# Kernel optimization log

Measured on AMD Instinct MI355X. Metric: run time of the kernel, lower is better.

Reference implementation:

```python
import jax, jax.numpy as jnp
import numpy as np

B, L = 2, 2048
D_MODEL, D_INNER, D_STATE, DT_RANK = 512, 1024, 16, 32
N_LAYERS, BLOCK, N_HEADS, CONV_K = 15, 64, 4, 4
VOCAB, D_OUT = 32000, 512


def setup_inputs() -> dict:
    key = jax.random.key(0)
    ks = iter(jax.random.split(key, 40))
    def nrm(shape, s=0.02):
        return jax.random.normal(next(ks), shape, dtype=jnp.float32) * s
    return {
        "tokens": jax.random.randint(next(ks), (B, L), 0, VOCAB, dtype=jnp.int32),
        "embed": nrm((VOCAB, D_MODEL)),
        "rms_w": jnp.ones((N_LAYERS, D_MODEL), jnp.float32),
        "W_in": nrm((N_LAYERS, D_MODEL, 2 * D_INNER)),
        "conv_w": nrm((N_LAYERS, D_INNER, CONV_K), 0.1),
        "conv_b": jnp.zeros((N_LAYERS, D_INNER), jnp.float32),
        "x_proj": nrm((N_LAYERS, D_INNER, DT_RANK + 2 * D_STATE)),
        "dt_w": nrm((N_LAYERS, DT_RANK, D_INNER), 0.1),
        "dt_b": jnp.full((N_LAYERS, D_INNER), -2.0, jnp.float32),
        "A_log": jnp.log(jnp.broadcast_to(jnp.arange(1, D_STATE + 1, dtype=jnp.float32), (N_LAYERS, D_INNER, D_STATE)) + 0.0),
        "D_skip": jnp.ones((N_LAYERS, D_INNER), jnp.float32),
        "W_out": nrm((N_LAYERS, D_INNER, D_MODEL)),
        "init_state": jnp.zeros((N_LAYERS, 1, 1, D_MODEL), jnp.float32),
        "Wq": nrm((D_MODEL, D_MODEL)), "Wk": nrm((D_MODEL, D_MODEL)), "Wv": nrm((D_MODEL, D_MODEL)),
        "bq": jnp.zeros((D_MODEL,), jnp.float32), "bk": jnp.zeros((D_MODEL,), jnp.float32), "bv": jnp.zeros((D_MODEL,), jnp.float32),
        "Wo_attn": nrm((D_MODEL, D_MODEL)), "bo": jnp.zeros((D_MODEL,), jnp.float32),
        "ln_w": jnp.ones((D_MODEL,), jnp.float32), "ln_b": jnp.zeros((D_MODEL,), jnp.float32),
        "head_w": nrm((D_MODEL, D_OUT)),
    }


def _silu(x):
    return x * jax.nn.sigmoid(x)


def _rmsnorm(x, w, eps=1e-6):
    return x * jax.lax.rsqrt(jnp.mean(x * x, axis=-1, keepdims=True) + eps) * w


def _mamba_block(h, Wi, cw, cb, xpw, dtw, dtb, Alog, Dsk, Wo):
    # h: (B, T, D) with T = BLOCK + 1 (state token prepended)
    Bb, T, _ = h.shape
    x, z = jnp.split(h @ Wi, 2, axis=-1)                      # (B,T,di) each
    xpad = jnp.pad(x, ((0, 0), (CONV_K - 1, 0), (0, 0)))      # causal depthwise conv
    x = sum(xpad[:, k:k + T, :] * cw[:, k] for k in range(CONV_K)) + cb
    x = _silu(x)
    xdbl = x @ xpw                                            # (B,T,dt_rank+2*ds)
    dt = jax.nn.softplus(xdbl[..., :DT_RANK] @ dtw + dtb)     # (B,T,di)
    Bt = xdbl[..., DT_RANK:DT_RANK + D_STATE]                 # (B,T,ds)
    Ct = xdbl[..., DT_RANK + D_STATE:]                        # (B,T,ds)
    A = -jnp.exp(Alog)                                        # (di,ds)

    def step(s, inp):
        dt_t, B_t, C_t, x_t = inp                             # (B,di),(B,ds),(B,ds),(B,di)
        s = s * jnp.exp(dt_t[..., None] * A) + (dt_t * x_t)[..., None] * B_t[:, None, :]
        return s, jnp.einsum('bds,bs->bd', s, C_t)

    s0 = jnp.zeros((Bb, D_INNER, D_STATE), x.dtype)
    xs = tuple(a.transpose(1, 0, 2) for a in (dt, Bt, Ct, x))  # time-major
    _, ys = jax.lax.scan(step, s0, xs)
    y = ys.transpose(1, 0, 2) + Dsk * x
    return (y * _silu(z)) @ Wo


def reference(tokens, embed, rms_w, W_in, conv_w, conv_b, x_proj, dt_w, dt_b,
              A_log, D_skip, W_out, init_state, Wq, Wk, Wv, bq, bk, bv,
              Wo_attn, bo, ln_w, ln_b, head_w):
    h = embed[tokens]                                          # (B,L,D)
    nB = L // BLOCK
    chunks = h.reshape(B, nB, BLOCK, D_MODEL).transpose(1, 0, 2, 3)  # (nB,B,bs,D)
    states0 = jnp.broadcast_to(init_state, (N_LAYERS, B, 1, D_MODEL)) + 0.0

    def block_step(states, chunk):
        co = chunk
        new_states = []
        for j in range(N_LAYERS):
            cwc = jnp.concatenate([states[j], _rmsnorm(co, rms_w[j])], axis=1)
            lo = _mamba_block(cwc, W_in[j], conv_w[j], conv_b[j], x_proj[j],
                              dt_w[j], dt_b[j], A_log[j], D_skip[j], W_out[j])
            new_states.append(jax.lax.stop_gradient(lo[:, -1:, :]))
            co = co + lo[:, 1:, :]
        ns = jnp.stack(new_states)
        return ns, (co, ns[-1][:, 0, :])

    _, (out_chunks, mem) = jax.lax.scan(block_step, states0, chunks)
    mamba_out = out_chunks.transpose(1, 0, 2, 3).reshape(B, L, D_MODEL)
    memory_bank = mem.transpose(1, 0, 2)                       # (B,nB,D)

    dh = D_MODEL // N_HEADS
    q = (mamba_out @ Wq.T + bq).reshape(B, L, N_HEADS, dh)
    k = (memory_bank @ Wk.T + bk).reshape(B, nB, N_HEADS, dh)
    v = (memory_bank @ Wv.T + bv).reshape(B, nB, N_HEADS, dh)
    tb = jnp.arange(L) // BLOCK
    allowed = jnp.arange(nB)[None, :] < tb[:, None]            # (L,nB) strictly-past blocks
    has_past = tb > 0
    mask = jnp.where(allowed | ~has_past[:, None], 0.0, -1e9)
    scores = jnp.einsum('blhd,bmhd->bhlm', q, k) / float(np.sqrt(dh)) + mask
    attn = jax.nn.softmax(scores, axis=-1)
    ao = jnp.einsum('bhlm,bmhd->blhd', attn, v).reshape(B, L, D_MODEL)
    ao = (ao @ Wo_attn.T + bo) * has_past.astype(mamba_out.dtype)[None, :, None]

    hres = mamba_out + ao
    mu = jnp.mean(hres, axis=-1, keepdims=True)
    var = jnp.var(hres, axis=-1, keepdims=True)
    hf = (hres - mu) * jax.lax.rsqrt(var + 1e-5) * ln_w + ln_b
    return hf @ head_w
```

## Files before the change

kernel.cpp:

```cpp
#include <hip/hip_runtime.h>
#include <hip/hip_cooperative_groups.h>

namespace cg = cooperative_groups;

typedef unsigned short u16;
typedef unsigned int u32;
typedef __attribute__((ext_vector_type(8))) short bf16x8;
typedef __attribute__((ext_vector_type(4))) float f32x4;

constexpr int BATCH = 2, SEQL = 2048, DMODEL = 512, DINNER = 1024;
constexpr int NLAYER = 15, BLKSZ = 64, NCHUNK = 32, TT = 65;

constexpr size_t OFF_H   = 0;
constexpr size_t OFF_ST  = 2097152;
constexpr size_t OFF_MEM = 2112512;
constexpr size_t OFF_XZ  = 2145280;
constexpr size_t OFF_XC  = 6138880;
constexpr size_t OFF_ANB = 8135680;
constexpr size_t OFF_XCB = 8688640;
constexpr size_t OFF_YMB = 9917440;
constexpr size_t OFF_WIT = 10900480;
constexpr size_t OFF_WOT = 18764800;
constexpr size_t OFF_XPT = 22696960;
constexpr size_t OFF_Q   = 2145280;
constexpr size_t OFF_K   = 4242432;
constexpr size_t OFF_V   = 4275200;
constexpr size_t OFF_AO  = 4307968;
constexpr size_t OFF_WTA = 6405120;

__device__ __forceinline__ u16 f2b(float f) {
  u32 u = __builtin_bit_cast(u32, f);
  u = (u + 0x7fffu + ((u >> 16) & 1u)) >> 16;
  return (u16)u;
}
__device__ __forceinline__ u32 pk2(float a, float b) {
  return (u32)f2b(a) | ((u32)f2b(b) << 16);
}

__global__ void __launch_bounds__(256,2)
wtrans_k(const float* __restrict__ src, u16* __restrict__ dst,
         int R, int C, int tiles_rc, int tc)
{
  __shared__ float tile[64*65];
  const int mat = blockIdx.x / tiles_rc;
  const int rem = blockIdx.x % tiles_rc;
  const int r0 = (rem / tc) * 64, c0 = (rem % tc) * 64;
  const float* s = src + (size_t)mat * R * C;
  u16* d = dst + (size_t)mat * C * R;
  for (int i = threadIdx.x; i < 4096; i += 256) {
    const int r = i >> 6, cc = i & 63;
    tile[r*65 + cc] = s[(size_t)(r0 + r)*C + c0 + cc];
  }
  __syncthreads();
  for (int i = threadIdx.x; i < 4096; i += 256) {
    const int ci = i >> 6, rr = i & 63;
    d[(size_t)(c0 + ci)*R + r0 + rr] = f2b(tile[rr*65 + ci]);
  }
}

__global__ void __launch_bounds__(256, 2)
mamba_coop(const int* __restrict__ tokens, const float* __restrict__ embed,
           const float* __restrict__ rms_w, const float* __restrict__ conv_w,
           const float* __restrict__ conv_b, const float* __restrict__ dt_w,
           const float* __restrict__ dt_b, const float* __restrict__ A_log,
           const float* __restrict__ D_skip, const float* __restrict__ init_state,
           float* __restrict__ ws)
{
  cg::grid_group grid = cg::this_grid();
  __shared__ __align__(16) float xd_lds[80*64];
  float* h_  = ws + OFF_H;
  float* st_ = ws + OFF_ST;
  float* memb = ws + OFF_MEM;
  const int NWG = gridDim.x;
  const int wg = blockIdx.x, tid = threadIdx.x;
  const int wv = tid >> 6, ln = tid & 63;
  const int lr = ln & 15, lq = ln >> 4;

  {
    const int gtid = wg*256 + tid;
    const int gstr = NWG*256;
    for (int g = gtid; g < BATCH*SEQL*(DMODEL/8); g += gstr) {
      const int bl = g >> 6;
      const int m0 = (g & 63) << 3;
      const int tok = tokens[bl];
      const float* ep = embed + (size_t)tok*DMODEL + m0;
      float* hp = h_ + (size_t)bl*DMODEL + m0;
      *(float4*)hp     = *(const float4*)ep;
      *(float4*)(hp+4) = *(const float4*)(ep+4);
    }
    for (int i = gtid; i < NLAYER*BATCH*DMODEL; i += gstr) {
      const int m = i & (DMODEL-1);
      const int j = i / (BATCH*DMODEL);
      st_[i] = init_state[j*DMODEL + m];
    }
  }
  grid.sync();

  for (int diag = 0; diag < NCHUNK + NLAYER - 1; ++diag) {
    const int c_lo = (diag - (NLAYER-1)) > 0 ? (diag - (NLAYER-1)) : 0;
    const int c_hi = diag < (NCHUNK-1) ? diag : (NCHUNK-1);
    const int nst = c_hi - c_lo + 1;
    const int sidx = wg % nst;
    const int swg  = wg / nst;
    const int nwg  = (NWG - 1 - sidx)/nst + 1;
    const int c = c_lo + sidx;
    const int j = diag - c;
    float* xz  = ws + OFF_XZ + (size_t)j*266240;
    float* xcf = ws + OFF_XC + (size_t)j*133120;
    u16* anb = (u16*)(ws + OFF_ANB) + (size_t)j*73728;
    u16* xcb = (u16*)(ws + OFF_XCB) + (size_t)j*163840;
    u16* ymb = (u16*)(ws + OFF_YMB) + (size_t)j*131072;
    const u16* WiT = (const u16*)(ws + OFF_WIT) + (size_t)j*1048576;
    const u16* WoT = (const u16*)(ws + OFF_WOT) + (size_t)j*524288;
    const u16* XpT = (const u16*)(ws + OFF_XPT) + (size_t)j*65536;
    const float* rw = rms_w + (size_t)j*DMODEL;

    {
      const int nwaves = nwg*4;
      for (int m = swg*4 + wv; m < 144; m += nwaves) {
        const int k0 = ln*8;
        uint4 pk;
        if (m < 130) {
          const int b = m/TT, t = m - b*TT;
          float v[8];
          if (t == 0) {
            const float* sp = st_ + ((size_t)j*BATCH + b)*DMODEL + k0;
            #pragma unroll
            for (int x = 0; x < 8; ++x) v[x] = sp[x];
          } else {
            const float* hp = h_ + (size_t)(b*SEQL + c*BLKSZ + t-1)*DMODEL + k0;
            const float4 v0 = *(const float4*)hp;
            const float4 v1 = *(const float4*)(hp+4);
            float ss = v0.x*v0.x + v0.y*v0.y + v0.z*v0.z + v0.w*v0.w
                     + v1.x*v1.x + v1.y*v1.y + v1.z*v1.z + v1.w*v1.w;
            #pragma unroll
            for (int off = 32; off > 0; off >>= 1) ss += __shfl_xor(ss, off);
            const float rs = rsqrtf(ss * (1.f/512.f) + 1e-6f);
            const float o[8] = {v0.x,v0.y,v0.z,v0.w,v1.x,v1.y,v1.z,v1.w};
            #pragma unroll
            for (int x = 0; x < 8; ++x) v[x] = o[x] * rs * rw[k0 + x];
          }
          pk = make_uint4(pk2(v[0],v[1]), pk2(v[2],v[3]), pk2(v[4],v[5]), pk2(v[6],v[7]));
        } else {
          pk = make_uint4(0,0,0,0);
        }
        *(uint4*)(anb + (size_t)m*512 + k0) = pk;
      }
    }
    grid.sync();

    {
      const float* cvb = conv_b + (size_t)j*DINNER;
      const float* cww = conv_w + (size_t)j*DINNER*4;
      for (int nb = swg; nb < 32; nb += nwg) {
        const int n_base = nb*64;
        f32x4 acc[3][4] = {};
        for (int kk = 0; kk < 16; ++kk) {
          const int k0 = kk*32 + lq*8;
          bf16x8 bf[4];
          #pragma unroll
          for (int nt = 0; nt < 4; ++nt)
            bf[nt] = *(const bf16x8*)(WiT + (size_t)(n_base + nt*16 + lr)*512 + k0);
          #pragma unroll
          for (int i = 0; i < 3; ++i) {
            if (i == 2 && wv != 0) continue;
            const int mt = wv + 4*i;
            const bf16x8 af = *(const bf16x8*)(anb + (size_t)(mt*16 + lr)*512 + k0);
            #pragma unroll
            for (int nt = 0; nt < 4; ++nt)
              acc[i][nt] = __builtin_amdgcn_mfma_f32_16x16x32_bf16(af, bf[nt], acc[i][nt], 0, 0, 0);
          }
        }
        #pragma unroll
        for (int i = 0; i < 3; ++i) {
          if (i == 2 && wv != 0) continue;
          const int mt = wv + 4*i;
          #pragma unroll
          for (int nt = 0; nt < 4; ++nt)
            #pragma unroll
            for (int r = 0; r < 4; ++r) {
              const int m = mt*16 + lq*4 + r;
              if (m < 130)
                xz[(size_t)m*2048 + n_base + nt*16 + lr] = acc[i][nt][r];
            }
        }
        if (nb < 16) {
          __syncthreads();
          for (int e = tid; e < 64*160; e += 256) {
            const int d = n_base + (e & 63);
            const int row2 = e >> 6;
            const int b = row2 / 80, t = row2 - b*80;
            if (t < TT) {
              const int m = b*TT + t;
              float a = cvb[d];
              #pragma unroll
              for (int q = 0; q < 4; ++q) {
                const int tt = t - 3 + q;
                if (tt >= 0) a = fmaf(xz[(size_t)(b*TT+tt)*2048 + d], cww[d*4+q], a);
              }
              const float sv = a / (1.f + __expf(-a));
              xcf[(size_t)m*1024 + d] = sv;
              xcb[(size_t)row2*1024 + d] = f2b(sv);
            } else {
              xcb[(size_t)row2*1024 + d] = 0;
            }
          }
        }
      }
    }
    grid.sync();

    if (swg < 8) {
      const int p = swg, b = p >> 2;
      const u16* xa = xcb + (size_t)b*80*1024;
      for (int mt = 0; mt < 5; ++mt) {
        f32x4 acc = {};
        for (int kk = 0; kk < 32; ++kk) {
          const int k0 = kk*32 + lq*8;
          const bf16x8 af = *(const bf16x8*)(xa + (size_t)(mt*16 + lr)*1024 + k0);
          const bf16x8 bf = *(const bf16x8*)(XpT + (size_t)(wv*16 + lr)*1024 + k0);
          acc = __builtin_amdgcn_mfma_f32_16x16x32_bf16(af, bf, acc, 0, 0, 0);
        }
        #pragma unroll
        for (int r = 0; r < 4; ++r)
          xd_lds[(mt*16 + lq*4 + r)*64 + wv*16 + lr] = acc[r];
      }
      __syncthreads();
      const int d = (p & 3)*256 + tid;
      float dtwr[32];
      const float* dwp = dt_w + (size_t)j*32*DINNER + d;
      #pragma unroll
      for (int r = 0; r < 32; ++r) dtwr[r] = dwp[(size_t)r*DINNER];
      float Ai[16], s[16];
      const float* alp = A_log + (size_t)j*DINNER*16 + (size_t)d*16;
      #pragma unroll
      for (int i = 0; i < 16; ++i) { Ai[i] = -__expf(alp[i]); s[i] = 0.f; }
      const float dtbv = dt_b[(size_t)j*DINNER + d];
      const float Dv   = D_skip[(size_t)j*DINNER + d];
      for (int t = 0; t < TT; ++t) {
        const float4* row = (const float4*)(xd_lds + t*64);
        float dl = dtbv;
        #pragma unroll
        for (int r = 0; r < 8; ++r) {
          const float4 x = row[r];
          dl = fmaf(x.x, dtwr[4*r+0], dl);
          dl = fmaf(x.y, dtwr[4*r+1], dl);
          dl = fmaf(x.z, dtwr[4*r+2], dl);
          dl = fmaf(x.w, dtwr[4*r+3], dl);
        }
        const float e = __expf(dl);
        const float dtv = (dl > 15.f) ? dl : log1pf(e);
        const float xcv = xcf[(size_t)(b*TT+t)*1024 + d];
        const float u = dtv * xcv;
        float yv = 0.f;
        #pragma unroll
        for (int i = 0; i < 4; ++i) {
          const float4 Bv = row[8+i];
          const float4 Cv = row[12+i];
          float P;
          P = __expf(dtv*Ai[4*i+0]); s[4*i+0] = fmaf(s[4*i+0], P, u*Bv.x); yv = fmaf(s[4*i+0], Cv.x, yv);
          P = __expf(dtv*Ai[4*i+1]); s[4*i+1] = fmaf(s[4*i+1], P, u*Bv.y); yv = fmaf(s[4*i+1], Cv.y, yv);
          P = __expf(dtv*Ai[4*i+2]); s[4*i+2] = fmaf(s[4*i+2], P, u*Bv.z); yv = fmaf(s[4*i+2], Cv.z, yv);
          P = __expf(dtv*Ai[4*i+3]); s[4*i+3] = fmaf(s[4*i+3], P, u*Bv.w); yv = fmaf(s[4*i+3], Cv.w, yv);
        }
        const float zv = xz[(size_t)(b*TT+t)*2048 + 1024 + d];
        const float sz = zv / (1.f + __expf(-zv));
        if (t >= 1)
          ymb[(size_t)(b*64 + t-1)*1024 + d] = f2b((yv + Dv*xcv) * sz);
      }
    }
    grid.sync();

    {
      for (int nt0 = swg; nt0 < 32; nt0 += nwg) {
        f32x4 acc[2] = {};
        for (int kk = 0; kk < 32; ++kk) {
          const int k0 = kk*32 + lq*8;
          const bf16x8 bf = *(const bf16x8*)(WoT + (size_t)(nt0*16 + lr)*1024 + k0);
          #pragma unroll
          for (int i = 0; i < 2; ++i) {
            const int mt = wv*2 + i;
            const bf16x8 af = *(const bf16x8*)(ymb + (size_t)(mt*16 + lr)*1024 + k0);
            acc[i] = __builtin_amdgcn_mfma_f32_16x16x32_bf16(af, bf, acc[i], 0, 0, 0);
          }
        }
        const int col = nt0*16 + lr;
        #pragma unroll
        for (int i = 0; i < 2; ++i) {
          const int mt = wv*2 + i;
          #pragma unroll
          for (int r = 0; r < 4; ++r) {
            const int m = mt*16 + lq*4 + r;
            const int b = m >> 6, tm = m & 63;
            const float v = acc[i][r];
            float* hp = h_ + (size_t)(b*SEQL + c*BLKSZ + tm)*DMODEL + col;
            *hp += v;
            if (tm == 63) {
              st_[((size_t)j*BATCH + b)*DMODEL + col] = v;
              if (j == NLAYER-1)
                memb[((size_t)b*NCHUNK + c)*DMODEL + col] = v;
            }
          }
        }
      }
    }
    grid.sync();
  }
}

__global__ void __launch_bounds__(256,1)
transpose_k(const float* __restrict__ wq, const float* __restrict__ wk,
            const float* __restrict__ wvm, const float* __restrict__ wo,
            float* __restrict__ ws)
{
  float* wt = ws + OFF_WTA;
  const float* srcs[4] = { wq, wk, wvm, wo };
  const int which = blockIdx.x >> 10;
  const int idx = ((blockIdx.x & 1023) << 8) + threadIdx.x;
  const int o = idx >> 9, m = idx & 511;
  wt[(size_t)which*262144 + (size_t)m*512 + o] = srcs[which][(size_t)o*512 + m];
}

__global__ void __launch_bounds__(256,1)
qkv_k(const float* __restrict__ bq, const float* __restrict__ bk, const float* __restrict__ bv,
      float* __restrict__ ws)
{
  __shared__ __align__(16) float lds[8192];
  const float* wt = ws + OFF_WTA;
  const int wg = blockIdx.x, tid = threadIdx.x;
  const int rtg = wg >> 2, ct = wg & 3;
  const float* A; const float* Bm; const float* bias; float* out; int m0;
  if (rtg < 256)      { A = ws+OFF_H;   Bm = wt;          bias = bq; out = ws+OFF_Q; m0 = rtg*16; }
  else if (rtg < 260) { A = ws+OFF_MEM; Bm = wt + 262144; bias = bk; out = ws+OFF_K; m0 = (rtg-256)*16; }
  else                { A = ws+OFF_MEM; Bm = wt + 524288; bias = bv; out = ws+OFF_V; m0 = (rtg-260)*16; }
  for (int i = tid; i < 2048; i += 256) {
    const int f = i*4;
    *(float4*)(lds+f) = *(const float4*)(A + (size_t)(m0 + (f>>9))*512 + (f & 511));
  }
  __syncthreads();
  const int col0 = ct*128 + (tid & 63)*2;
  const int rq = tid >> 6;
  const float2* wp2 = (const float2*)(Bm + col0);
  const float* ap = lds + rq*2048;
  float acc0[4] = {0,0,0,0}, acc1[4] = {0,0,0,0};
  for (int k = 0; k < 512; k += 4) {
    const float2 w0 = wp2[(size_t)(k+0)*256];
    const float2 w1 = wp2[(size_t)(k+1)*256];
    const float2 w2 = wp2[(size_t)(k+2)*256];
    const float2 w3 = wp2[(size_t)(k+3)*256];
    #pragma unroll
    for (int r4 = 0; r4 < 4; ++r4) {
      const float4 a = *(const float4*)(ap + r4*512 + k);
      acc0[r4] = fmaf(a.x, w0.x, acc0[r4]); acc1[r4] = fmaf(a.x, w0.y, acc1[r4]);
      acc0[r4] = fmaf(a.y, w1.x, acc0[r4]); acc1[r4] = fmaf(a.y, w1.y, acc1[r4]);
      acc0[r4] = fmaf(a.z, w2.x, acc0[r4]); acc1[r4] = fmaf(a.z, w2.y, acc1[r4]);
      acc0[r4] = fmaf(a.w, w3.x, acc0[r4]); acc1[r4] = fmaf(a.w, w3.y, acc1[r4]);
    }
  }
  const float bb0 = bias[col0], bb1 = bias[col0+1];
  #pragma unroll
  for (int r4 = 0; r4 < 4; ++r4)
    *(float2*)(out + (size_t)(m0 + rq*4 + r4)*512 + col0) = make_float2(acc0[r4]+bb0, acc1[r4]+bb1);
}

__global__ void __launch_bounds__(256,1)
attn_k(float* __restrict__ ws)
{
  const float* q  = ws + OFF_Q;
  const float* kk = ws + OFF_K;
  const float* vvv = ws + OFF_V;
  float* ao = ws + OFF_AO;
  const int gw = (blockIdx.x*256 + threadIdx.x) >> 6;
  const int ln = threadIdx.x & 63;
  const int l = gw & (SEQL-1);
  const int bh = gw >> 11;
  const int b = bh >> 2, hh = bh & 3;
  const int tb = l >> 6;
  float* aop = ao + (size_t)(b*SEQL + l)*512 + hh*128;
  if (tb == 0) { *(float2*)(aop + ln*2) = make_float2(0.f, 0.f); return; }
  float sc = -1e30f;
  if (ln < tb) {
    const float* qp = q + (size_t)(b*SEQL+l)*512 + hh*128;
    const float* kp = kk + (size_t)(b*NCHUNK+ln)*512 + hh*128;
    float s = 0.f;
    for (int dd = 0; dd < 128; dd += 4) {
      const float4 qq = *(const float4*)(qp+dd);
      const float4 kv = *(const float4*)(kp+dd);
      s += qq.x*kv.x + qq.y*kv.y + qq.z*kv.z + qq.w*kv.w;
    }
    sc = s * 0.08838834764831845f;
  }
  float mx = sc;
  #pragma unroll
  for (int off = 32; off > 0; off >>= 1) mx = fmaxf(mx, __shfl_xor(mx, off));
  const float w = (ln < tb) ? __expf(sc - mx) : 0.f;
  float sm = w;
  #pragma unroll
  for (int off = 32; off > 0; off >>= 1) sm += __shfl_xor(sm, off);
  const float inv = 1.f / sm;
  float a0 = 0.f, a1 = 0.f;
  const int d0 = ln*2;
  for (int mm = 0; mm < tb; ++mm) {
    const float am = __shfl(w, mm) * inv;
    const float2 vp = *(const float2*)(vvv + (size_t)(b*NCHUNK+mm)*512 + hh*128 + d0);
    a0 = fmaf(am, vp.x, a0);
    a1 = fmaf(am, vp.y, a1);
  }
  *(float2*)(aop + d0) = make_float2(a0, a1);
}

__global__ void __launch_bounds__(256,1)
outproj_k(const float* __restrict__ bo, float* __restrict__ ws)
{
  __shared__ __align__(16) float lds[8192];
  float* ao  = ws + OFF_AO;
  const float* woT = ws + OFF_WTA + 786432;
  const float* h_ = ws + OFF_H;
  const int wg = blockIdx.x, tid = threadIdx.x;
  const int rtg = wg >> 2, ct = wg & 3;
  const int m0 = rtg*16;
  for (int i = tid; i < 2048; i += 256) {
    const int f = i*4;
    *(float4*)(lds+f) = *(const float4*)(ao + (size_t)(m0 + (f>>9))*512 + (f & 511));
  }
  __syncthreads();
  const int col0 = ct*128 + (tid & 63)*2;
  const int rq = tid >> 6;
  const float2* wp2 = (const float2*)(woT + col0);
  const float* ap = lds + rq*2048;
  float acc0[4] = {0,0,0,0}, acc1[4] = {0,0,0,0};
  for (int k = 0; k < 512; k += 4) {
    const float2 w0 = wp2[(size_t)(k+0)*256];
    const float2 w1 = wp2[(size_t)(k+1)*256];
    const float2 w2 = wp2[(size_t)(k+2)*256];
    const float2 w3 = wp2[(size_t)(k+3)*256];
    #pragma unroll
    for (int r4 = 0; r4 < 4; ++r4) {
      const float4 a = *(const float4*)(ap + r4*512 + k);
      acc0[r4] = fmaf(a.x, w0.x, acc0[r4]); acc1[r4] = fmaf(a.x, w0.y, acc1[r4]);
      acc0[r4] = fmaf(a.y, w1.x, acc0[r4]); acc1[r4] = fmaf(a.y, w1.y, acc1[r4]);
      acc0[r4] = fmaf(a.z, w2.x, acc0[r4]); acc1[r4] = fmaf(a.z, w2.y, acc1[r4]);
      acc0[r4] = fmaf(a.w, w3.x, acc0[r4]); acc1[r4] = fmaf(a.w, w3.y, acc1[r4]);
    }
  }
  const float bb0 = bo[col0], bb1 = bo[col0+1];
  #pragma unroll
  for (int r4 = 0; r4 < 4; ++r4) {
    const int m = m0 + rq*4 + r4;
    const float hp = ((m & (SEQL-1)) >= BLKSZ) ? 1.f : 0.f;
    const float2 hv = *(const float2*)(h_ + (size_t)m*512 + col0);
    *(float2*)(ao + (size_t)m*512 + col0) =
        make_float2(hv.x + (acc0[r4]+bb0)*hp, hv.y + (acc1[r4]+bb1)*hp);
  }
}

__global__ void __launch_bounds__(256,1)
lnhead_k(const float* __restrict__ lnw, const float* __restrict__ lnb,
         const float* __restrict__ head_w, float* __restrict__ ws, float* __restrict__ out)
{
  __shared__ __align__(16) float lds[8192];
  const float* hres = ws + OFF_AO;
  const int wg = blockIdx.x, tid = threadIdx.x;
  const int wv = tid >> 6, ln = tid & 63;
  const int rtg = wg >> 2, ct = wg & 3;
  const int m0 = rtg*16;
  for (int r = wv; r < 16; r += 4) {
    const float* src = hres + (size_t)(m0+r)*512 + ln*8;
    const float4 v0 = *(const float4*)src;
    const float4 v1 = *(const float4*)(src+4);
    float s1 = v0.x+v0.y+v0.z+v0.w + v1.x+v1.y+v1.z+v1.w;
    float s2 = v0.x*v0.x+v0.y*v0.y+v0.z*v0.z+v0.w*v0.w
             + v1.x*v1.x+v1.y*v1.y+v1.z*v1.z+v1.w*v1.w;
    #pragma unroll
    for (int off = 32; off > 0; off >>= 1) { s1 += __shfl_xor(s1, off); s2 += __shfl_xor(s2, off); }
    const float mu = s1 * (1.f/512.f);
    const float var = fmaxf(s2 * (1.f/512.f) - mu*mu, 0.f);
    const float nf = rsqrtf(var + 1e-5f);
    const float o[8] = {v0.x,v0.y,v0.z,v0.w,v1.x,v1.y,v1.z,v1.w};
    #pragma unroll
    for (int x = 0; x < 8; ++x)
      lds[r*512 + ln*8 + x] = (o[x]-mu)*nf*lnw[ln*8+x] + lnb[ln*8+x];
  }
  __syncthreads();
  const int col0 = ct*128 + (tid & 63)*2;
  const int rq = tid >> 6;
  const float2* wp2 = (const float2*)(head_w + col0);
  const float* ap = lds + rq*2048;
  float acc0[4] = {0,0,0,0}, acc1[4] = {0,0,0,0};
  for (int k = 0; k < 512; k += 4) {
    const float2 w0 = wp2[(size_t)(k+0)*256];
    const float2 w1 = wp2[(size_t)(k+1)*256];
    const float2 w2 = wp2[(size_t)(k+2)*256];
    const float2 w3 = wp2[(size_t)(k+3)*256];
    #pragma unroll
    for (int r4 = 0; r4 < 4; ++r4) {
      const float4 a = *(const float4*)(ap + r4*512 + k);
      acc0[r4] = fmaf(a.x, w0.x, acc0[r4]); acc1[r4] = fmaf(a.x, w0.y, acc1[r4]);
      acc0[r4] = fmaf(a.y, w1.x, acc0[r4]); acc1[r4] = fmaf(a.y, w1.y, acc1[r4]);
      acc0[r4] = fmaf(a.z, w2.x, acc0[r4]); acc1[r4] = fmaf(a.z, w2.y, acc1[r4]);
      acc0[r4] = fmaf(a.w, w3.x, acc0[r4]); acc1[r4] = fmaf(a.w, w3.y, acc1[r4]);
    }
  }
  #pragma unroll
  for (int r4 = 0; r4 < 4; ++r4) {
    const size_t oi = (size_t)(m0 + rq*4 + r4)*512 + col0;
    *(float2*)(out + oi) = make_float2(acc0[r4], acc1[r4]);
  }
}

extern "C" void kernel_launch(void* const* d_in, const int* in_sizes, int n_in,
                              void* d_out, int out_size, void* d_ws, size_t ws_size,
                              hipStream_t stream)
{
  const int*   tokens     = (const int*)d_in[0];
  const float* embed      = (const float*)d_in[1];
  const float* rms_w      = (const float*)d_in[2];
  const float* W_in       = (const float*)d_in[3];
  const float* conv_w     = (const float*)d_in[4];
  const float* conv_b     = (const float*)d_in[5];
  const float* x_proj     = (const float*)d_in[6];
  const float* dt_w       = (const float*)d_in[7];
  const float* dt_b       = (const float*)d_in[8];
  const float* A_log      = (const float*)d_in[9];
  const float* D_skip     = (const float*)d_in[10];
  const float* W_out      = (const float*)d_in[11];
  const float* init_state = (const float*)d_in[12];
  const float* Wq         = (const float*)d_in[13];
  const float* Wk         = (const float*)d_in[14];
  const float* Wv         = (const float*)d_in[15];
  const float* bq         = (const float*)d_in[16];
  const float* bk         = (const float*)d_in[17];
  const float* bv         = (const float*)d_in[18];
  const float* Wo_attn    = (const float*)d_in[19];
  const float* bo         = (const float*)d_in[20];
  const float* ln_w       = (const float*)d_in[21];
  const float* ln_b       = (const float*)d_in[22];
  const float* head_w     = (const float*)d_in[23];
  float* ws = (float*)d_ws;
  float* out = (float*)d_out;

  hipLaunchKernelGGL(wtrans_k, dim3(15*8*32), dim3(256), 0, stream,
                     W_in, (u16*)(ws + OFF_WIT), 512, 2048, 8*32, 32);
  hipLaunchKernelGGL(wtrans_k, dim3(15*16*8), dim3(256), 0, stream,
                     W_out, (u16*)(ws + OFF_WOT), 1024, 512, 16*8, 8);
  hipLaunchKernelGGL(wtrans_k, dim3(15*16*1), dim3(256), 0, stream,
                     x_proj, (u16*)(ws + OFF_XPT), 1024, 64, 16*1, 1);

  int occ = 1;
  (void)hipOccupancyMaxActiveBlocksPerMultiprocessor(&occ, mamba_coop, 256, 0);
  if (occ < 1) occ = 1;
  if (occ > 2) occ = 2;
  const int grid = 256 * occ;

  void* args[] = { (void*)&tokens, (void*)&embed, (void*)&rms_w,
                   (void*)&conv_w, (void*)&conv_b, (void*)&dt_w,
                   (void*)&dt_b, (void*)&A_log, (void*)&D_skip,
                   (void*)&init_state, (void*)&ws };
  hipLaunchCooperativeKernel(reinterpret_cast<const void*>(&mamba_coop),
                             dim3(grid), dim3(256), args, 0, stream);

  hipLaunchKernelGGL(transpose_k, dim3(4096), dim3(256), 0, stream, Wq, Wk, Wv, Wo_attn, ws);
  hipLaunchKernelGGL(qkv_k, dim3(1056), dim3(256), 0, stream, bq, bk, bv, ws);
  hipLaunchKernelGGL(attn_k, dim3(4096), dim3(256), 0, stream, ws);
  hipLaunchKernelGGL(outproj_k, dim3(1024), dim3(256), 0, stream, bo, ws);
  hipLaunchKernelGGL(lnhead_k, dim3(1024), dim3(256), 0, stream, ln_w, ln_b, head_w, ws, out);
}
```

Before: 15.94 ms.

## Replace grid-wide syncs with per-layer workgroup groups and flag-based dataflow

```diff
diff --git a/kernel.cpp b/kernel.cpp
--- a/kernel.cpp
+++ b/kernel.cpp
@@ -1,7 +1,4 @@
 #include <hip/hip_runtime.h>
-#include <hip/hip_cooperative_groups.h>
-
-namespace cg = cooperative_groups;
 
 typedef unsigned short u16;
 typedef unsigned int u32;
@@ -10,18 +7,20 @@
 
 constexpr int BATCH = 2, SEQL = 2048, DMODEL = 512, DINNER = 1024;
 constexpr int NLAYER = 15, BLKSZ = 64, NCHUNK = 32, TT = 65;
+constexpr int NWG = 480;
 
 constexpr size_t OFF_H   = 0;
 constexpr size_t OFF_ST  = 2097152;
 constexpr size_t OFF_MEM = 2112512;
 constexpr size_t OFF_XZ  = 2145280;
-constexpr size_t OFF_XC  = 6138880;
-constexpr size_t OFF_ANB = 8135680;
-constexpr size_t OFF_XCB = 8688640;
-constexpr size_t OFF_YMB = 9917440;
-constexpr size_t OFF_WIT = 10900480;
-constexpr size_t OFF_WOT = 18764800;
-constexpr size_t OFF_XPT = 22696960;
+constexpr size_t OFF_ANB = 6138880;
+constexpr size_t OFF_XCB = 6691840;
+constexpr size_t OFF_YMB = 7920640;
+constexpr size_t OFF_WIT = 8903680;
+constexpr size_t OFF_WOT = 16768000;
+constexpr size_t OFF_XPT = 20700160;
+constexpr size_t OFF_DTW = 21191680;
+constexpr size_t OFF_FLG = 21437440;
 constexpr size_t OFF_Q   = 2145280;
 constexpr size_t OFF_K   = 4242432;
 constexpr size_t OFF_V   = 4275200;
@@ -33,8 +32,34 @@
   u = (u + 0x7fffu + ((u >> 16) & 1u)) >> 16;
   return (u16)u;
 }
+__device__ __forceinline__ float b2f(u16 u) {
+  u32 v = ((u32)u) << 16;
+  return __builtin_bit_cast(float, v);
+}
 __device__ __forceinline__ u32 pk2(float a, float b) {
   return (u32)f2b(a) | ((u32)f2b(b) << 16);
+}
+
+__device__ __forceinline__ void spin_until(int* f, int target) {
+  int k = 0;
+  while (__hip_atomic_load(f, __ATOMIC_RELAXED, __HIP_MEMORY_SCOPE_AGENT) < target) {
+    __builtin_amdgcn_s_sleep(8);
+    if (((++k) & 255) == 0)
+      (void)__hip_atomic_load(f, __ATOMIC_ACQUIRE, __HIP_MEMORY_SCOPE_AGENT);
+  }
+  (void)__hip_atomic_load(f, __ATOMIC_ACQUIRE, __HIP_MEMORY_SCOPE_AGENT);
+}
+__device__ __forceinline__ void wait_flag(int* f, int target) {
+  if (threadIdx.x == 0) spin_until(f, target);
+  __syncthreads();
+}
+__device__ __forceinline__ void stage_bar(int* f, int target, bool arrive) {
+  __syncthreads();
+  if (threadIdx.x == 0) {
+    if (arrive) __hip_atomic_fetch_add(f, 1, __ATOMIC_RELEASE, __HIP_MEMORY_SCOPE_AGENT);
+    spin_until(f, target);
+  }
+  __syncthreads();
 }
 
 __global__ void __launch_bounds__(256,2)
@@ -58,23 +83,32 @@
   }
 }
 
+__global__ void __launch_bounds__(256,2)
+dtwtrans_k(const float* __restrict__ src, u16* __restrict__ dst)
+{
+  const int i = blockIdx.x*256 + threadIdx.x;
+  const int jj = i >> 15, rem = i & 32767;
+  const int d = rem >> 5, r = rem & 31;
+  dst[i] = f2b(src[(size_t)jj*32768 + (size_t)r*1024 + d]);
+}
+
 __global__ void __launch_bounds__(256, 2)
 mamba_coop(const int* __restrict__ tokens, const float* __restrict__ embed,
            const float* __restrict__ rms_w, const float* __restrict__ conv_w,
-           const float* __restrict__ conv_b, const float* __restrict__ dt_w,
-           const float* __restrict__ dt_b, const float* __restrict__ A_log,
-           const float* __restrict__ D_skip, const float* __restrict__ init_state,
-           float* __restrict__ ws)
-{
-  cg::grid_group grid = cg::this_grid();
+           const float* __restrict__ conv_b, const float* __restrict__ dt_b,
+           const float* __restrict__ A_log, const float* __restrict__ D_skip,
+           const float* __restrict__ init_state, float* __restrict__ ws)
+{
   __shared__ __align__(16) float xd_lds[80*64];
   float* h_  = ws + OFF_H;
   float* st_ = ws + OFF_ST;
   float* memb = ws + OFF_MEM;
-  const int NWG = gridDim.x;
+  int* FLG = (int*)(ws + OFF_FLG);
   const int wg = blockIdx.x, tid = threadIdx.x;
   const int wv = tid >> 6, ln = tid & 63;
   const int lr = ln & 15, lq = ln >> 4;
+  const int j = wg >> 5;
+  const int swg = wg & 31;
 
   {
     const int gtid = wg*256 + tid;
@@ -90,128 +124,117 @@
     }
     for (int i = gtid; i < NLAYER*BATCH*DMODEL; i += gstr) {
       const int m = i & (DMODEL-1);
-      const int j = i / (BATCH*DMODEL);
-      st_[i] = init_state[j*DMODEL + m];
-    }
-  }
-  grid.sync();
-
-  for (int diag = 0; diag < NCHUNK + NLAYER - 1; ++diag) {
-    const int c_lo = (diag - (NLAYER-1)) > 0 ? (diag - (NLAYER-1)) : 0;
-    const int c_hi = diag < (NCHUNK-1) ? diag : (NCHUNK-1);
-    const int nst = c_hi - c_lo + 1;
-    const int sidx = wg % nst;
-    const int swg  = wg / nst;
-    const int nwg  = (NWG - 1 - sidx)/nst + 1;
-    const int c = c_lo + sidx;
-    const int j = diag - c;
-    float* xz  = ws + OFF_XZ + (size_t)j*266240;
-    float* xcf = ws + OFF_XC + (size_t)j*133120;
-    u16* anb = (u16*)(ws + OFF_ANB) + (size_t)j*73728;
-    u16* xcb = (u16*)(ws + OFF_XCB) + (size_t)j*163840;
-    u16* ymb = (u16*)(ws + OFF_YMB) + (size_t)j*131072;
-    const u16* WiT = (const u16*)(ws + OFF_WIT) + (size_t)j*1048576;
-    const u16* WoT = (const u16*)(ws + OFF_WOT) + (size_t)j*524288;
-    const u16* XpT = (const u16*)(ws + OFF_XPT) + (size_t)j*65536;
-    const float* rw = rms_w + (size_t)j*DMODEL;
+      const int jj = i / (BATCH*DMODEL);
+      st_[i] = init_state[jj*DMODEL + m];
+    }
+  }
+  stage_bar(FLG + 30720, NWG, true);
+
+  float* xz  = ws + OFF_XZ + (size_t)j*266240;
+  u16* anb = (u16*)(ws + OFF_ANB) + (size_t)j*73728;
+  u16* xcb = (u16*)(ws + OFF_XCB) + (size_t)j*163840;
+  u16* ymb = (u16*)(ws + OFF_YMB) + (size_t)j*131072;
+  const u16* WiT = (const u16*)(ws + OFF_WIT) + (size_t)j*1048576;
+  const u16* WoT = (const u16*)(ws + OFF_WOT) + (size_t)j*524288;
+  const u16* XpT = (const u16*)(ws + OFF_XPT) + (size_t)j*65536;
+  const u16* DwT = (const u16*)(ws + OFF_DTW) + (size_t)j*32768;
+  const float* rw = rms_w + (size_t)j*DMODEL;
+  const float* cvb = conv_b + (size_t)j*DINNER;
+  const float* cww = conv_w + (size_t)j*DINNER*4;
+
+  for (int c = 0; c < NCHUNK; ++c) {
+    int* fs = FLG + ((c*15 + j)*4)*16;
+    if (j > 0) wait_flag(FLG + ((c*15 + j-1)*4 + 3)*16, 32);
+
+    for (int m = swg*4 + wv; m < 144; m += 128) {
+      const int k0 = ln*8;
+      uint4 pk;
+      if (m < 130) {
+        const int b = m/TT, t = m - b*TT;
+        float v[8];
+        if (t == 0) {
+          const float* sp = st_ + ((size_t)j*BATCH + b)*DMODEL + k0;
+          #pragma unroll
+          for (int x = 0; x < 8; ++x) v[x] = sp[x];
+        } else {
+          const float* hp = h_ + (size_t)(b*SEQL + c*BLKSZ + t-1)*DMODEL + k0;
+          const float4 v0 = *(const float4*)hp;
+          const float4 v1 = *(const float4*)(hp+4);
+          float ss = v0.x*v0.x + v0.y*v0.y + v0.z*v0.z + v0.w*v0.w
+                   + v1.x*v1.x + v1.y*v1.y + v1.z*v1.z + v1.w*v1.w;
+          #pragma unroll
+          for (int off = 32; off > 0; off >>= 1) ss += __shfl_xor(ss, off);
+          const float rs = rsqrtf(ss * (1.f/512.f) + 1e-6f);
+          const float o[8] = {v0.x,v0.y,v0.z,v0.w,v1.x,v1.y,v1.z,v1.w};
+          #pragma unroll
+          for (int x = 0; x < 8; ++x) v[x] = o[x] * rs * rw[k0 + x];
+        }
+        pk = make_uint4(pk2(v[0],v[1]), pk2(v[2],v[3]), pk2(v[4],v[5]), pk2(v[6],v[7]));
+      } else {
+        pk = make_uint4(0,0,0,0);
+      }
+      *(uint4*)(anb + (size_t)m*512 + k0) = pk;
+    }
+    stage_bar(fs + 0*16, 32, true);
 
     {
-      const int nwaves = nwg*4;
-      for (int m = swg*4 + wv; m < 144; m += nwaves) {
-        const int k0 = ln*8;
-        uint4 pk;
-        if (m < 130) {
-          const int b = m/TT, t = m - b*TT;
-          float v[8];
-          if (t == 0) {
-            const float* sp = st_ + ((size_t)j*BATCH + b)*DMODEL + k0;
-            #pragma unroll
-            for (int x = 0; x < 8; ++x) v[x] = sp[x];
-          } else {
-            const float* hp = h_ + (size_t)(b*SEQL + c*BLKSZ + t-1)*DMODEL + k0;
-            const float4 v0 = *(const float4*)hp;
-            const float4 v1 = *(const float4*)(hp+4);
-            float ss = v0.x*v0.x + v0.y*v0.y + v0.z*v0.z + v0.w*v0.w
-                     + v1.x*v1.x + v1.y*v1.y + v1.z*v1.z + v1.w*v1.w;
-            #pragma unroll
-            for (int off = 32; off > 0; off >>= 1) ss += __shfl_xor(ss, off);
-            const float rs = rsqrtf(ss * (1.f/512.f) + 1e-6f);
-            const float o[8] = {v0.x,v0.y,v0.z,v0.w,v1.x,v1.y,v1.z,v1.w};
-            #pragma unroll
-            for (int x = 0; x < 8; ++x) v[x] = o[x] * rs * rw[k0 + x];
-          }
-          pk = make_uint4(pk2(v[0],v[1]), pk2(v[2],v[3]), pk2(v[4],v[5]), pk2(v[6],v[7]));
-        } else {
-          pk = make_uint4(0,0,0,0);
-        }
-        *(uint4*)(anb + (size_t)m*512 + k0) = pk;
-      }
-    }
-    grid.sync();
-
-    {
-      const float* cvb = conv_b + (size_t)j*DINNER;
-      const float* cww = conv_w + (size_t)j*DINNER*4;
-      for (int nb = swg; nb < 32; nb += nwg) {
-        const int n_base = nb*64;
-        f32x4 acc[3][4] = {};
-        for (int kk = 0; kk < 16; ++kk) {
-          const int k0 = kk*32 + lq*8;
-          bf16x8 bf[4];
-          #pragma unroll
-          for (int nt = 0; nt < 4; ++nt)
-            bf[nt] = *(const bf16x8*)(WiT + (size_t)(n_base + nt*16 + lr)*512 + k0);
-          #pragma unroll
-          for (int i = 0; i < 3; ++i) {
-            if (i == 2 && wv != 0) continue;
-            const int mt = wv + 4*i;
-            const bf16x8 af = *(const bf16x8*)(anb + (size_t)(mt*16 + lr)*512 + k0);
-            #pragma unroll
-            for (int nt = 0; nt < 4; ++nt)
-              acc[i][nt] = __builtin_amdgcn_mfma_f32_16x16x32_bf16(af, bf[nt], acc[i][nt], 0, 0, 0);
-          }
-        }
+      const int nb = swg;
+      const int n_base = nb*64;
+      f32x4 acc[3][4] = {};
+      for (int kk = 0; kk < 16; ++kk) {
+        const int k0 = kk*32 + lq*8;
+        bf16x8 bf[4];
+        #pragma unroll
+        for (int nt = 0; nt < 4; ++nt)
+          bf[nt] = *(const bf16x8*)(WiT + (size_t)(n_base + nt*16 + lr)*512 + k0);
         #pragma unroll
         for (int i = 0; i < 3; ++i) {
           if (i == 2 && wv != 0) continue;
           const int mt = wv + 4*i;
+          const bf16x8 af = *(const bf16x8*)(anb + (size_t)(mt*16 + lr)*512 + k0);
           #pragma unroll
           for (int nt = 0; nt < 4; ++nt)
+            acc[i][nt] = __builtin_amdgcn_mfma_f32_16x16x32_bf16(af, bf[nt], acc[i][nt], 0, 0, 0);
+        }
+      }
+      #pragma unroll
+      for (int i = 0; i < 3; ++i) {
+        if (i == 2 && wv != 0) continue;
+        const int mt = wv + 4*i;
+        #pragma unroll
+        for (int nt = 0; nt < 4; ++nt)
+          #pragma unroll
+          for (int r = 0; r < 4; ++r) {
+            const int m = mt*16 + lq*4 + r;
+            if (m < 130)
+              xz[(size_t)m*2048 + n_base + nt*16 + lr] = acc[i][nt][r];
+          }
+      }
+      if (nb < 16) {
+        __syncthreads();
+        for (int e = tid; e < 64*160; e += 256) {
+          const int d = n_base + (e & 63);
+          const int row2 = e >> 6;
+          const int b = row2 / 80, t = row2 - b*80;
+          if (t < TT) {
+            float a = cvb[d];
             #pragma unroll
-            for (int r = 0; r < 4; ++r) {
-              const int m = mt*16 + lq*4 + r;
-              if (m < 130)
-                xz[(size_t)m*2048 + n_base + nt*16 + lr] = acc[i][nt][r];
+            for (int q = 0; q < 4; ++q) {
+              const int tt = t - 3 + q;
+              if (tt >= 0) a = fmaf(xz[(size_t)(b*TT+tt)*2048 + d], cww[d*4+q], a);
             }
-        }
-        if (nb < 16) {
-          __syncthreads();
-          for (int e = tid; e < 64*160; e += 256) {
-            const int d = n_base + (e & 63);
-            const int row2 = e >> 6;
-            const int b = row2 / 80, t = row2 - b*80;
-            if (t < TT) {
-              const int m = b*TT + t;
-              float a = cvb[d];
-              #pragma unroll
-              for (int q = 0; q < 4; ++q) {
-                const int tt = t - 3 + q;
-                if (tt >= 0) a = fmaf(xz[(size_t)(b*TT+tt)*2048 + d], cww[d*4+q], a);
-              }
-              const float sv = a / (1.f + __expf(-a));
-              xcf[(size_t)m*1024 + d] = sv;
-              xcb[(size_t)row2*1024 + d] = f2b(sv);
-            } else {
-              xcb[(size_t)row2*1024 + d] = 0;
-            }
+            const float sv = a / (1.f + __expf(-a));
+            xcb[(size_t)row2*1024 + d] = f2b(sv);
+          } else {
+            xcb[(size_t)row2*1024 + d] = 0;
           }
         }
       }
     }
-    grid.sync();
+    stage_bar(fs + 1*16, 32, true);
 
     if (swg < 8) {
-      const int p = swg, b = p >> 2;
+      const int p = swg, b = p >> 2, slice = p & 3;
       const u16* xa = xcb + (size_t)b*80*1024;
       for (int mt = 0; mt < 5; ++mt) {
         f32x4 acc = {};
@@ -226,85 +249,98 @@
           xd_lds[(mt*16 + lq*4 + r)*64 + wv*16 + lr] = acc[r];
       }
       __syncthreads();
-      const int d = (p & 3)*256 + tid;
-      float dtwr[32];
-      const float* dwp = dt_w + (size_t)j*32*DINNER + d;
-      #pragma unroll
-      for (int r = 0; r < 32; ++r) dtwr[r] = dwp[(size_t)r*DINNER];
-      float Ai[16], s[16];
-      const float* alp = A_log + (size_t)j*DINNER*16 + (size_t)d*16;
-      #pragma unroll
-      for (int i = 0; i < 16; ++i) { Ai[i] = -__expf(alp[i]); s[i] = 0.f; }
-      const float dtbv = dt_b[(size_t)j*DINNER + d];
-      const float Dv   = D_skip[(size_t)j*DINNER + d];
-      for (int t = 0; t < TT; ++t) {
-        const float4* row = (const float4*)(xd_lds + t*64);
-        float dl = dtbv;
+      for (int ni = 0; ni < 4; ++ni) {
+        const int n0 = (slice*16 + wv*4 + ni)*16;
+        const bf16x8 bf = *(const bf16x8*)(DwT + (size_t)(n0 + lr)*32 + lq*8);
+        const float dtbv_l = dt_b[(size_t)j*DINNER + n0 + lr];
+        for (int mt = 0; mt < 5; ++mt) {
+          bf16x8 af;
+          #pragma unroll
+          for (int x = 0; x < 8; ++x)
+            af[x] = (short)f2b(xd_lds[(mt*16 + lr)*64 + lq*8 + x]);
+          f32x4 acc = {};
+          acc = __builtin_amdgcn_mfma_f32_16x16x32_bf16(af, bf, acc, 0, 0, 0);
+          #pragma unroll
+          for (int r = 0; r < 4; ++r) {
+            const int m = mt*16 + lq*4 + r;
+            if (m < TT) {
+              const float v = acc[r] + dtbv_l;
+              const float sp = (v > 15.f) ? v : log1pf(__expf(v));
+              xz[((size_t)b*TT + m)*2048 + n0 + lr] = sp;
+            }
+          }
+        }
+      }
+      __syncthreads();
+      {
+        const int d = slice*256 + tid;
+        float Ai[16], s[16];
+        const float* alp = A_log + (size_t)j*DINNER*16 + (size_t)d*16;
         #pragma unroll
-        for (int r = 0; r < 8; ++r) {
-          const float4 x = row[r];
-          dl = fmaf(x.x, dtwr[4*r+0], dl);
-          dl = fmaf(x.y, dtwr[4*r+1], dl);
-          dl = fmaf(x.z, dtwr[4*r+2], dl);
-          dl = fmaf(x.w, dtwr[4*r+3], dl);
-        }
-        const float e = __expf(dl);
-        const float dtv = (dl > 15.f) ? dl : log1pf(e);
-        const float xcv = xcf[(size_t)(b*TT+t)*1024 + d];
-        const float u = dtv * xcv;
-        float yv = 0.f;
-        #pragma unroll
-        for (int i = 0; i < 4; ++i) {
-          const float4 Bv = row[8+i];
-          const float4 Cv = row[12+i];
-          float P;
-          P = __expf(dtv*Ai[4*i+0]); s[4*i+0] = fmaf(s[4*i+0], P, u*Bv.x); yv = fmaf(s[4*i+0], Cv.x, yv);
-          P = __expf(dtv*Ai[4*i+1]); s[4*i+1] = fmaf(s[4*i+1], P, u*Bv.y); yv = fmaf(s[4*i+1], Cv.y, yv);
-          P = __expf(dtv*Ai[4*i+2]); s[4*i+2] = fmaf(s[4*i+2], P, u*Bv.z); yv = fmaf(s[4*i+2], Cv.z, yv);
-          P = __expf(dtv*Ai[4*i+3]); s[4*i+3] = fmaf(s[4*i+3], P, u*Bv.w); yv = fmaf(s[4*i+3], Cv.w, yv);
-        }
-        const float zv = xz[(size_t)(b*TT+t)*2048 + 1024 + d];
-        const float sz = zv / (1.f + __expf(-zv));
-        if (t >= 1)
-          ymb[(size_t)(b*64 + t-1)*1024 + d] = f2b((yv + Dv*xcv) * sz);
-      }
-    }
-    grid.sync();
+        for (int i = 0; i < 16; ++i) { Ai[i] = -__expf(alp[i]); s[i] = 0.f; }
+        const float Dv = D_skip[(size_t)j*DINNER + d];
+        const float* dtp = xz + (size_t)b*TT*2048 + d;
+        const u16*   xcp = xcb + (size_t)b*80*1024 + d;
+        const float* xzp = xz + (size_t)b*TT*2048 + 1024 + d;
+        u16* ymp = ymb + (size_t)b*64*1024 + d;
+        for (int t = 0; t < TT; ++t) {
+          const float dt_ = dtp[(size_t)t*2048];
+          const float xcv = b2f(xcp[(size_t)t*1024]);
+          const float zv  = xzp[(size_t)t*2048];
+          const float u = dt_ * xcv;
+          const float4* row = (const float4*)(xd_lds + t*64 + 32);
+          float y0 = 0.f, y1 = 0.f, y2 = 0.f, y3 = 0.f;
+          #pragma unroll
+          for (int i = 0; i < 4; ++i) {
+            const float4 Bv = row[i];
+            const float4 Cv = row[4+i];
+            float P;
+            P = __expf(dt_*Ai[4*i+0]); s[4*i+0] = fmaf(s[4*i+0], P, u*Bv.x); y0 = fmaf(s[4*i+0], Cv.x, y0);
+            P = __expf(dt_*Ai[4*i+1]); s[4*i+1] = fmaf(s[4*i+1], P, u*Bv.y); y1 = fmaf(s[4*i+1], Cv.y, y1);
+            P = __expf(dt_*Ai[4*i+2]); s[4*i+2] = fmaf(s[4*i+2], P, u*Bv.z); y2 = fmaf(s[4*i+2], Cv.z, y2);
+            P = __expf(dt_*Ai[4*i+3]); s[4*i+3] = fmaf(s[4*i+3], P, u*Bv.w); y3 = fmaf(s[4*i+3], Cv.w, y3);
+          }
+          const float sz = zv / (1.f + __expf(-zv));
+          if (t >= 1)
+            ymp[(size_t)(t-1)*1024] = f2b(((y0+y1)+(y2+y3) + Dv*xcv) * sz);
+        }
+      }
+    }
+    stage_bar(fs + 2*16, 8, swg < 8);
 
     {
-      for (int nt0 = swg; nt0 < 32; nt0 += nwg) {
-        f32x4 acc[2] = {};
-        for (int kk = 0; kk < 32; ++kk) {
-          const int k0 = kk*32 + lq*8;
-          const bf16x8 bf = *(const bf16x8*)(WoT + (size_t)(nt0*16 + lr)*1024 + k0);
-          #pragma unroll
-          for (int i = 0; i < 2; ++i) {
-            const int mt = wv*2 + i;
-            const bf16x8 af = *(const bf16x8*)(ymb + (size_t)(mt*16 + lr)*1024 + k0);
-            acc[i] = __builtin_amdgcn_mfma_f32_16x16x32_bf16(af, bf, acc[i], 0, 0, 0);
-          }
-        }
-        const int col = nt0*16 + lr;
+      const int nt0 = swg;
+      f32x4 acc[2] = {};
+      for (int kk = 0; kk < 32; ++kk) {
+        const int k0 = kk*32 + lq*8;
+        const bf16x8 bf = *(const bf16x8*)(WoT + (size_t)(nt0*16 + lr)*1024 + k0);
         #pragma unroll
         for (int i = 0; i < 2; ++i) {
           const int mt = wv*2 + i;
-          #pragma unroll
-          for (int r = 0; r < 4; ++r) {
-            const int m = mt*16 + lq*4 + r;
-            const int b = m >> 6, tm = m & 63;
-            const float v = acc[i][r];
-            float* hp = h_ + (size_t)(b*SEQL + c*BLKSZ + tm)*DMODEL + col;
-            *hp += v;
-            if (tm == 63) {
-              st_[((size_t)j*BATCH + b)*DMODEL + col] = v;
-              if (j == NLAYER-1)
-                memb[((size_t)b*NCHUNK + c)*DMODEL + col] = v;
-            }
+          const bf16x8 af = *(const bf16x8*)(ymb + (size_t)(mt*16 + lr)*1024 + k0);
+          acc[i] = __builtin_amdgcn_mfma_f32_16x16x32_bf16(af, bf, acc[i], 0, 0, 0);
+        }
+      }
+      const int col = nt0*16 + lr;
+      #pragma unroll
+      for (int i = 0; i < 2; ++i) {
+        const int mt = wv*2 + i;
+        #pragma unroll
+        for (int r = 0; r < 4; ++r) {
+          const int m = mt*16 + lq*4 + r;
+          const int b = m >> 6, tm = m & 63;
+          const float v = acc[i][r];
+          float* hp = h_ + (size_t)(b*SEQL + c*BLKSZ + tm)*DMODEL + col;
+          *hp += v;
+          if (tm == 63) {
+            st_[((size_t)j*BATCH + b)*DMODEL + col] = v;
+            if (j == NLAYER-1)
+              memb[((size_t)b*NCHUNK + c)*DMODEL + col] = v;
           }
         }
       }
     }
-    grid.sync();
+    stage_bar(fs + 3*16, 32, true);
   }
 }
 
@@ -545,19 +581,22 @@
                      W_out, (u16*)(ws + OFF_WOT), 1024, 512, 16*8, 8);
   hipLaunchKernelGGL(wtrans_k, dim3(15*16*1), dim3(256), 0, stream,
                      x_proj, (u16*)(ws + OFF_XPT), 1024, 64, 16*1, 1);
-
-  int occ = 1;
-  (void)hipOccupancyMaxActiveBlocksPerMultiprocessor(&occ, mamba_coop, 256, 0);
-  if (occ < 1) occ = 1;
-  if (occ > 2) occ = 2;
-  const int grid = 256 * occ;
+  hipLaunchKernelGGL(dtwtrans_k, dim3(15*128), dim3(256), 0, stream,
+                     dt_w, (u16*)(ws + OFF_DTW));
+
+  (void)hipMemsetAsync(ws + OFF_FLG, 0, (30720 + 64) * sizeof(int), stream);
 
   void* args[] = { (void*)&tokens, (void*)&embed, (void*)&rms_w,
-                   (void*)&conv_w, (void*)&conv_b, (void*)&dt_w,
-                   (void*)&dt_b, (void*)&A_log, (void*)&D_skip,
-                   (void*)&init_state, (void*)&ws };
-  hipLaunchCooperativeKernel(reinterpret_cast<const void*>(&mamba_coop),
-                             dim3(grid), dim3(256), args, 0, stream);
+                   (void*)&conv_w, (void*)&conv_b, (void*)&dt_b,
+                   (void*)&A_log, (void*)&D_skip, (void*)&init_state, (void*)&ws };
+  hipError_t cerr = hipLaunchCooperativeKernel(
+      reinterpret_cast<const void*>(&mamba_coop),
+      dim3(NWG), dim3(256), args, 0, stream);
+  if (cerr != hipSuccess) {
+    hipLaunchKernelGGL(mamba_coop, dim3(NWG), dim3(256), 0, stream,
+                       tokens, embed, rms_w, conv_w, conv_b, dt_b,
+                       A_log, D_skip, init_state, ws);
+  }
 
   hipLaunchKernelGGL(transpose_k, dim3(4096), dim3(256), 0, stream, Wq, Wk, Wv, Wo_attn, ws);
   hipLaunchKernelGGL(qkv_k, dim3(1056), dim3(256), 0, stream, bq, bk, bv, ws);
```

Measured after the change: 14.49 ms. -9.1%, faster.
